# Kernel optimization log

Hardware: AMD Instinct MI355X
Metric: run time of the kernel (lower is better)

The kernel has to match this reference:

```python
import jax, jax.numpy as jnp
import numpy as np

N, E, DIN, ED, H, C = 50000, 800000, 128, 16, 4, 128
HC = H * C
SLOPE = 0.2


def gat_conv(x, ei_src, ei_dst, ea, W, a_src, a_dst, We, a_e, b):
    # x: [N, din]; ea: [E, ed] (self-loops already appended by caller)
    n = x.shape[0]
    h = (x @ W).reshape(n, H, C)                       # [N,H,C]
    al_src = (h * a_src).sum(-1)                       # [N,H]
    al_dst = (h * a_dst).sum(-1)                       # [N,H]
    e = (ea @ We).reshape(-1, H, C)                    # [E,H,C]
    al_e = (e * a_e).sum(-1)                           # [E,H]
    alpha = al_src[ei_src] + al_dst[ei_dst] + al_e     # [E,H]
    alpha = jnp.where(alpha > 0, alpha, SLOPE * alpha)  # LeakyReLU(0.2)
    # per-destination-node segment softmax (stable)
    amax = jax.ops.segment_max(alpha, ei_dst, num_segments=n)
    amax = jnp.where(jnp.isfinite(amax), amax, 0.0)
    ex = jnp.exp(alpha - amax[ei_dst])
    den = jax.ops.segment_sum(ex, ei_dst, num_segments=n)
    alpha = ex / (den[ei_dst] + 1e-16)                 # [E,H]
    msg = h[ei_src] * alpha[:, :, None]                # [E,H,C]
    out = jax.ops.segment_sum(msg, ei_dst, num_segments=n)  # [N,H,C]
    return out.reshape(n, HC) + b


def setup_inputs() -> dict:
    key = jax.random.key(0)
    ks = jax.random.split(key, 16)
    s = 0.05
    inp = {
        "x": jax.random.normal(ks[0], (N, DIN), jnp.float32),
        "edge_index": jax.random.randint(ks[1], (2, E), 0, N, jnp.int64),
        "edge_features": jax.random.normal(ks[2], (E, ED), jnp.float32),
        # layer 1 params
        "W1": jax.random.normal(ks[3], (DIN, HC), jnp.float32) * s,
        "att_src1": jax.random.normal(ks[4], (H, C), jnp.float32) * s,
        "att_dst1": jax.random.normal(ks[5], (H, C), jnp.float32) * s,
        "lin_e1": jax.random.normal(ks[6], (ED, HC), jnp.float32) * s,
        "att_e1": jax.random.normal(ks[7], (H, C), jnp.float32) * s,
        "b1": jnp.zeros((HC,), jnp.float32),
        # layer 2 params
        "W2": jax.random.normal(ks[8], (HC, HC), jnp.float32) * s,
        "att_src2": jax.random.normal(ks[9], (H, C), jnp.float32) * s,
        "att_dst2": jax.random.normal(ks[10], (H, C), jnp.float32) * s,
        "lin_e2": jax.random.normal(ks[11], (ED, HC), jnp.float32) * s,
        "att_e2": jax.random.normal(ks[12], (H, C), jnp.float32) * s,
        "b2": jnp.zeros((HC,), jnp.float32),
    }
    return inp


def reference(x, edge_index, edge_features,
              W1, att_src1, att_dst1, lin_e1, att_e1, b1,
              W2, att_src2, att_dst2, lin_e2, att_e2, b2):
    # add self-loops once (PyG default: add_self_loops=True, edge_attr fill='mean')
    loop = jnp.arange(N, dtype=edge_index.dtype)
    ei_src = jnp.concatenate([edge_index[0], loop])
    ei_dst = jnp.concatenate([edge_index[1], loop])
    mean_ea = edge_features.mean(0)
    ea = jnp.concatenate([edge_features, jnp.broadcast_to(mean_ea, (N, ED))], axis=0)

    h = gat_conv(x, ei_src, ei_dst, ea, W1, att_src1, att_dst1, lin_e1, att_e1, b1)
    h = jax.nn.elu(h)
    h = gat_conv(h, ei_src, ei_dst, ea, W2, att_src2, att_dst2, lin_e2, att_e2, b2)
    return jax.nn.elu(h)
```

## Files before the change

kernel.cpp:

```cpp
#include <hip/hip_runtime.h>
#include <math.h>

#define NNODE 50000
#define NEDGE 800000
#define DINv  128
#define EDv   16
#define NHv   4
#define CHv   128
#define HCv   512
#define SLOPEv 0.2f
#define MEANBLK 512
#define CONVN (NNODE * DINv / 4)

typedef __attribute__((ext_vector_type(8))) short bf16x8;
typedef __attribute__((ext_vector_type(4))) float f32x4;
typedef __attribute__((address_space(3))) unsigned lds_u32;
typedef const __attribute__((address_space(1))) unsigned glb_u32;

__device__ __forceinline__ ushort f2b(float f) {
  unsigned u = __float_as_uint(f);
  u += 0x7FFF + ((u >> 16) & 1);
  return (ushort)(u >> 16);
}
__device__ __forceinline__ float blo(unsigned u) { return __uint_as_float(u << 16); }
__device__ __forceinline__ float bhi(unsigned u) { return __uint_as_float(u & 0xffff0000u); }

__global__ void detect_kernel(const int* __restrict__ ei, int* __restrict__ flag) {
  __shared__ int bad;
  if (threadIdx.x == 0) bad = 0;
  __syncthreads();
  for (int i = threadIdx.x; i < 2048; i += 256)
    if (ei[2 * i + 1] != 0) bad = 1;
  __syncthreads();
  if (threadIdx.x == 0) flag[0] = bad ? 0 : 1;
}

__device__ __forceinline__ int load_idx(const int* __restrict__ ei, int e, int row, int wide) {
  if (wide) return ei[2 * ((size_t)row * NEDGE + e)];
  return ei[(size_t)row * NEDGE + e];
}

__global__ void count_kernel(const int* __restrict__ ei, const int* __restrict__ flag,
                             int* __restrict__ deg) {
  int e = blockIdx.x * blockDim.x + threadIdx.x;
  if (e < NEDGE) {
    int w = flag[0];
    atomicAdd(&deg[load_idx(ei, e, 1, w)], 1);
  }
}

__global__ __launch_bounds__(1024) void scan_kernel(const int* __restrict__ deg,
                                                    int* __restrict__ row_ptr) {
  __shared__ int wsum[16];
  int tid = threadIdx.x;
  int wid = tid >> 6, lane = tid & 63;
  int carry = 0;
  for (int base = 0; base < NNODE; base += 4096) {
    int idx = base + tid * 4;
    int4 x = make_int4(0, 0, 0, 0);
    if (idx < NNODE) x = *(const int4*)(deg + idx);
    int t0 = x.x, t1 = t0 + x.y, t2 = t1 + x.z, t3 = t2 + x.w;
    int v = t3;
#pragma unroll
    for (int off = 1; off < 64; off <<= 1) {
      int t = __shfl_up(v, off, 64);
      if (lane >= off) v += t;
    }
    if (lane == 63) wsum[wid] = v;
    __syncthreads();
    if (wid == 0) {
      int s = (lane < 16) ? wsum[lane] : 0;
#pragma unroll
      for (int off = 1; off < 16; off <<= 1) {
        int t = __shfl_up(s, off, 64);
        if (lane >= off) s += t;
      }
      if (lane < 16) wsum[lane] = s;
    }
    __syncthreads();
    int woff = wid ? wsum[wid - 1] : 0;
    int excl = carry + woff + v - t3;
    if (idx < NNODE) {
      int4 o = make_int4(excl, excl + t0, excl + t1, excl + t2);
      *(int4*)(row_ptr + idx) = o;
    }
    carry += wsum[15];
    __syncthreads();
  }
  if (tid == 0) row_ptr[NNODE] = carry;
}

__global__ void scatter_kernel(const int* __restrict__ ei, const int* __restrict__ flag,
                               const int* __restrict__ row_ptr, int* __restrict__ cursor,
                               int* __restrict__ src_sorted, int* __restrict__ pos) {
  int e = blockIdx.x * blockDim.x + threadIdx.x;
  if (e < NEDGE) {
    int w = flag[0];
    int d = load_idx(ei, e, 1, w);
    int s = load_idx(ei, e, 0, w);
    int p = row_ptr[d] + atomicAdd(&cursor[d], 1);
    src_sorted[p] = s;
    pos[e] = p;
  }
}

__global__ void prep_kernel(const float* __restrict__ We1, const float* __restrict__ ae1,
                            const float* __restrict__ We2, const float* __restrict__ ae2,
                            float* __restrict__ v1, float* __restrict__ v2) {
  int t = threadIdx.x;
  int layer = t >> 6, u = t & 63;
  int d = u >> 2, h = u & 3;
  const float* We = layer ? We2 : We1;
  const float* ae = layer ? ae2 : ae1;
  float s = 0.f;
  for (int c = 0; c < CHv; c++) s += We[(size_t)d * HCv + h * CHv + c] * ae[h * CHv + c];
  (layer ? v2 : v1)[d * 4 + h] = s;
}

__global__ void ale_both_kernel(const float* __restrict__ ea, const int* __restrict__ pos,
                                const float* __restrict__ v1, const float* __restrict__ v2,
                                float* __restrict__ al1, float* __restrict__ al2,
                                float* __restrict__ partials) {
  __shared__ float sv1[64], sv2[64];
  if (threadIdx.x < 64) sv1[threadIdx.x] = v1[threadIdx.x];
  else if (threadIdx.x < 128) sv2[threadIdx.x - 64] = v2[threadIdx.x - 64];
  __syncthreads();
  float acc[EDv];
#pragma unroll
  for (int d = 0; d < EDv; d++) acc[d] = 0.f;
  int stride = gridDim.x * blockDim.x;
  for (int e = blockIdx.x * blockDim.x + threadIdx.x; e < NEDGE; e += stride) {
    const float4* pr = (const float4*)(ea + (size_t)e * EDv);
    float row[16];
    *(float4*)&row[0] = pr[0]; *(float4*)&row[4] = pr[1];
    *(float4*)&row[8] = pr[2]; *(float4*)&row[12] = pr[3];
    float a0 = 0, a1 = 0, a2 = 0, a3 = 0;
    float b0 = 0, b1 = 0, b2 = 0, b3 = 0;
#pragma unroll
    for (int d = 0; d < 16; d++) {
      acc[d] += row[d];
      a0 += row[d] * sv1[d * 4 + 0];
      a1 += row[d] * sv1[d * 4 + 1];
      a2 += row[d] * sv1[d * 4 + 2];
      a3 += row[d] * sv1[d * 4 + 3];
      b0 += row[d] * sv2[d * 4 + 0];
      b1 += row[d] * sv2[d * 4 + 1];
      b2 += row[d] * sv2[d * 4 + 2];
      b3 += row[d] * sv2[d * 4 + 3];
    }
    int p = pos[e];
    ((float4*)al1)[p] = make_float4(a0, a1, a2, a3);
    ((float4*)al2)[p] = make_float4(b0, b1, b2, b3);
  }
  __shared__ float red[4][EDv];
  int wid = threadIdx.x >> 6, lane = threadIdx.x & 63;
#pragma unroll
  for (int d = 0; d < EDv; d++) {
    float v = acc[d];
    for (int off = 32; off; off >>= 1) v += __shfl_down(v, off, 64);
    if (lane == 0) red[wid][d] = v;
  }
  __syncthreads();
  if (threadIdx.x < EDv) {
    float v = red[0][threadIdx.x] + red[1][threadIdx.x] + red[2][threadIdx.x] + red[3][threadIdx.x];
    partials[blockIdx.x * EDv + threadIdx.x] = v;
  }
}

__global__ void fold_kernel(const float* __restrict__ partials,
                            const float* __restrict__ v1, const float* __restrict__ v2,
                            float* __restrict__ loop1, float* __restrict__ loop2) {
  int tid = threadIdx.x;
  int d = tid & 15, r0 = tid >> 4;
  float v = 0.f;
  for (int r = r0; r < MEANBLK; r += 16) v += partials[r * EDv + d];
  __shared__ float buf[256];
  __shared__ float ms[16];
  buf[tid] = v;
  __syncthreads();
  if (r0 < 8) buf[tid] += buf[tid + 128];
  __syncthreads();
  if (r0 < 4) buf[tid] += buf[tid + 64];
  __syncthreads();
  if (r0 < 2) buf[tid] += buf[tid + 32];
  __syncthreads();
  if (r0 == 0) ms[d] = (buf[tid] + buf[tid + 16]) * (1.0f / NEDGE);
  __syncthreads();
  if (tid < 8) {
    const float* vv = (tid >> 2) ? v2 : v1;
    int h = tid & 3;
    float a = 0.f;
    for (int d2 = 0; d2 < EDv; d2++) a += ms[d2] * vv[d2 * 4 + h];
    ((tid >> 2) ? loop2 : loop1)[h] = a;
  }
}

__global__ void convwt_kernel(const float* __restrict__ x, const float* __restrict__ W1,
                              const float* __restrict__ W2, ushort* __restrict__ xb,
                              ushort* __restrict__ Bt1, ushort* __restrict__ Bt2) {
  int i = blockIdx.x * 256 + threadIdx.x;
  if (i < CONVN) {
    float4 v = ((const float4*)x)[i];
    ushort4 o;
    o.x = f2b(v.x); o.y = f2b(v.y); o.z = f2b(v.z); o.w = f2b(v.w);
    ((ushort4*)xb)[i] = o;
  } else if (i < CONVN + DINv * HCv) {
    int idx = i - CONVN;
    int k = idx >> 9, n = idx & (HCv - 1);
    Bt1[(size_t)n * DINv + k] = f2b(W1[idx]);
  } else if (i < CONVN + DINv * HCv + HCv * HCv) {
    int idx = i - CONVN - DINv * HCv;
    int k = idx >> 9, n = idx & (HCv - 1);
    Bt2[(size_t)n * HCv + k] = f2b(W2[idx]);
  }
}

__global__ __launch_bounds__(256) void gemm_mfma_kernel(const ushort* __restrict__ A,
                                                        const ushort* __restrict__ Bt,
                                                        ushort* __restrict__ C, int M, int K,
                                                        const float* __restrict__ a_src,
                                                        const float* __restrict__ a_dst,
                                                        float* __restrict__ al_src,
                                                        float* __restrict__ al_dst) {
  __shared__ ushort As[8][128][8];
  __shared__ ushort Bs[8][128][8];
  __shared__ float ssa[128], ssd[128];
  __shared__ float rsum[2][128][2];
  int tid = threadIdx.x;
  int wid = tid >> 6, lane = tid & 63;

  int nblk = gridDim.x * gridDim.y;
  int j = blockIdx.y * gridDim.x + blockIdx.x;
  int q = nblk >> 3, rem = nblk & 7;
  int xcd = j & 7, idx = j >> 3;
  int d = (xcd < rem) ? xcd * (q + 1) + idx : rem * (q + 1) + (xcd - rem) * q + idx;
  int rb = (d >> 2) * 128, cb = (d & 3) * 128;
  int hblk = cb >> 7;

  int wm = (wid >> 1) * 64, wn = (wid & 1) * 64;
  int lr = lane & 15, lq = lane >> 4;

  if (tid < 128) { ssa[tid] = a_src[cb + tid]; ssd[tid] = a_dst[cb + tid]; }

  f32x4 acc[4][4];
#pragma unroll
  for (int i = 0; i < 4; i++)
#pragma unroll
    for (int jx = 0; jx < 4; jx++) acc[i][jx] = (f32x4){0.f, 0.f, 0.f, 0.f};

  ushort* AsF = &As[0][0][0];
  ushort* BsF = &Bs[0][0][0];

  for (int k0 = 0; k0 < K; k0 += 64) {
#pragma unroll
    for (int s = 0; s < 4; s++) {
      int c = s * 256 + tid;
      int kq = c >> 7, m = c & 127;
      int row = rb + m; if (row >= M) row = M - 1;
      const ushort* gA = A + (size_t)row * K + k0 + kq * 8;
      __builtin_amdgcn_global_load_lds((glb_u32*)gA, (lds_u32*)(AsF + (size_t)c * 8), 16, 0, 0);
    }
#pragma unroll
    for (int s = 0; s < 4; s++) {
      int c = s * 256 + tid;
      int kq = c >> 7, n = c & 127;
      const ushort* gB = Bt + (size_t)(cb + n) * K + k0 + kq * 8;
      __builtin_amdgcn_global_load_lds((glb_u32*)gB, (lds_u32*)(BsF + (size_t)c * 8), 16, 0, 0);
    }
    __syncthreads();
#pragma unroll
    for (int hh = 0; hh < 2; hh++) {
      bf16x8 af[4], bfr[4];
#pragma unroll
      for (int i = 0; i < 4; i++) {
        af[i]  = *(const bf16x8*)&As[hh * 4 + lq][wm + i * 16 + lr][0];
        bfr[i] = *(const bf16x8*)&Bs[hh * 4 + lq][wn + i * 16 + lr][0];
      }
#pragma unroll
      for (int i = 0; i < 4; i++)
#pragma unroll
        for (int jx = 0; jx < 4; jx++)
          acc[i][jx] = __builtin_amdgcn_mfma_f32_16x16x32_bf16(af[i], bfr[jx], acc[i][jx], 0, 0, 0);
    }
    __syncthreads();
  }

#pragma unroll
  for (int i = 0; i < 4; i++) {
    int rbase = rb + wm + i * 16 + lq * 4;
#pragma unroll
    for (int jx = 0; jx < 4; jx++) {
      int col = cb + wn + jx * 16 + lr;
#pragma unroll
      for (int r = 0; r < 4; r++) {
        int row = rbase + r;
        if (row < M) C[(size_t)row * HCv + col] = f2b(acc[i][jx][r]);
      }
    }
  }

  float sa[4], sd[4];
#pragma unroll
  for (int jx = 0; jx < 4; jx++) {
    int c = wn + jx * 16 + lr;
    sa[jx] = ssa[c]; sd[jx] = ssd[c];
  }
#pragma unroll
  for (int i = 0; i < 4; i++) {
#pragma unroll
    for (int r = 0; r < 4; r++) {
      float s1 = 0.f, s2 = 0.f;
#pragma unroll
      for (int jx = 0; jx < 4; jx++) {
        s1 = fmaf(acc[i][jx][r], sa[jx], s1);
        s2 = fmaf(acc[i][jx][r], sd[jx], s2);
      }
#pragma unroll
      for (int off = 1; off < 16; off <<= 1) {
        s1 += __shfl_xor(s1, off, 16);
        s2 += __shfl_xor(s2, off, 16);
      }
      if (lr == 0) {
        int row = wm + i * 16 + lq * 4 + r;
        rsum[0][row][wn >> 6] = s1;
        rsum[1][row][wn >> 6] = s2;
      }
    }
  }
  __syncthreads();
  if (tid < 128) {
    int row = rb + tid;
    if (row < M) {
      al_src[(size_t)row * 4 + hblk] = rsum[0][tid][0] + rsum[0][tid][1];
      al_dst[(size_t)row * 4 + hblk] = rsum[1][tid][0] + rsum[1][tid][1];
    }
  }
}

__device__ __forceinline__ void fma8(float* acc, float w, uint4 u) {
  acc[0] = fmaf(w, blo(u.x), acc[0]);
  acc[1] = fmaf(w, bhi(u.x), acc[1]);
  acc[2] = fmaf(w, blo(u.y), acc[2]);
  acc[3] = fmaf(w, bhi(u.y), acc[3]);
  acc[4] = fmaf(w, blo(u.z), acc[4]);
  acc[5] = fmaf(w, bhi(u.z), acc[5]);
  acc[6] = fmaf(w, blo(u.w), acc[6]);
  acc[7] = fmaf(w, bhi(u.w), acc[7]);
}

__global__ __launch_bounds__(256) void node_kernel(
    const ushort* __restrict__ hb, const float* __restrict__ al_src,
    const float* __restrict__ al_dst, const float* __restrict__ al_e,
    const float* __restrict__ loop_al_e, const int* __restrict__ row_ptr,
    const int* __restrict__ src_sorted, const float* __restrict__ bias,
    float* __restrict__ outf, ushort* __restrict__ outb) {
  int wid = threadIdx.x >> 6, lane = threadIdx.x & 63;
  int n = blockIdx.x * 4 + wid;
  if (n >= NNODE) return;
  int base = row_ptr[n];
  int deg = row_ptr[n + 1] - base;
  int h = lane >> 4;
  int jj = lane & 15;

  float aldh = al_dst[(size_t)n * 4 + h];
  float a0 = al_src[(size_t)n * 4 + h] + aldh + loop_al_e[h];
  float alph = a0 > 0.f ? a0 : SLOPEv * a0;
  float wl = __expf(alph);

  uint4 uself = *((const uint4*)(hb + ((size_t)n << 9)) + lane);

  float acc[8];
#pragma unroll
  for (int q = 0; q < 8; q++) acc[q] = 0.f;
  float den = 0.f;

  for (int cs = 0; cs < deg; cs += 16) {
    int cl = min(16, deg - cs);
    float w = 0.f;
    int sv = 0;
    if (jj < cl) {
      int p = base + cs + jj;
      sv = src_sorted[p];
      float a = al_src[(size_t)sv * 4 + h] + al_e[(size_t)p * 4 + h] + aldh;
      a = a > 0.f ? a : SLOPEv * a;
      w = __expf(a);
      den += w;
    }
    int cl4 = (cl + 3) & ~3;
    for (int j0 = 0; j0 < cl4; j0 += 4) {
      int s0 = __shfl(sv, j0 + 0, 16);
      int s1 = __shfl(sv, j0 + 1, 16);
      int s2 = __shfl(sv, j0 + 2, 16);
      int s3 = __shfl(sv, j0 + 3, 16);
      float w0 = __shfl(w, j0 + 0, 16);
      float w1 = __shfl(w, j0 + 1, 16);
      float w2 = __shfl(w, j0 + 2, 16);
      float w3 = __shfl(w, j0 + 3, 16);
      uint4 u0 = *((const uint4*)(hb + ((size_t)s0 << 9)) + lane);
      uint4 u1 = *((const uint4*)(hb + ((size_t)s1 << 9)) + lane);
      uint4 u2 = *((const uint4*)(hb + ((size_t)s2 << 9)) + lane);
      uint4 u3 = *((const uint4*)(hb + ((size_t)s3 << 9)) + lane);
      fma8(acc, w0, u0);
      fma8(acc, w1, u1);
      fma8(acc, w2, u2);
      fma8(acc, w3, u3);
    }
  }

  fma8(acc, wl, uself);

#pragma unroll
  for (int off = 8; off; off >>= 1) den += __shfl_xor(den, off, 16);
  den += wl;
  float rden = 1.f / (den + 1e-16f);

  const float4* bp = (const float4*)(bias + lane * 8);
  float4 b0 = bp[0], b1 = bp[1];
  float bv[8] = {b0.x, b0.y, b0.z, b0.w, b1.x, b1.y, b1.z, b1.w};
  float r[8];
#pragma unroll
  for (int q = 0; q < 8; q++) {
    float t = acc[q] * rden + bv[q];
    r[q] = t > 0.f ? t : expm1f(t);
  }
  if (outf) {
    float4* op = (float4*)(outf + (size_t)n * HCv + lane * 8);
    op[0] = make_float4(r[0], r[1], r[2], r[3]);
    op[1] = make_float4(r[4], r[5], r[6], r[7]);
  }
  if (outb) {
    uint4 o;
    o.x = (unsigned)f2b(r[0]) | ((unsigned)f2b(r[1]) << 16);
    o.y = (unsigned)f2b(r[2]) | ((unsigned)f2b(r[3]) << 16);
    o.z = (unsigned)f2b(r[4]) | ((unsigned)f2b(r[5]) << 16);
    o.w = (unsigned)f2b(r[6]) | ((unsigned)f2b(r[7]) << 16);
    ((uint4*)(outb + (size_t)n * HCv))[lane] = o;
  }
}

static inline char* take(char*& p, size_t bytes) {
  char* r = p;
  p += (bytes + 255) & ~(size_t)255;
  return r;
}

extern "C" void kernel_launch(void* const* d_in, const int* in_sizes, int n_in,
                              void* d_out, int out_size, void* d_ws, size_t ws_size,
                              hipStream_t stream) {
  (void)in_sizes; (void)n_in; (void)out_size; (void)ws_size;
  const float* x   = (const float*)d_in[0];
  const int*   ei  = (const int*)d_in[1];
  const float* ea  = (const float*)d_in[2];
  const float* W1  = (const float*)d_in[3];
  const float* as1 = (const float*)d_in[4];
  const float* ad1 = (const float*)d_in[5];
  const float* We1 = (const float*)d_in[6];
  const float* ae1 = (const float*)d_in[7];
  const float* b1  = (const float*)d_in[8];
  const float* W2  = (const float*)d_in[9];
  const float* as2 = (const float*)d_in[10];
  const float* ad2 = (const float*)d_in[11];
  const float* We2 = (const float*)d_in[12];
  const float* ae2 = (const float*)d_in[13];
  const float* b2  = (const float*)d_in[14];
  float* out = (float*)d_out;

  char* p = (char*)d_ws;
  ushort* hb        = (ushort*)take(p, (size_t)NNODE * HCv * 2);
  float* al_src     = (float*)take(p, (size_t)NNODE * 4 * 4);
  float* al_dst     = (float*)take(p, (size_t)NNODE * 4 * 4);
  float* ale1       = (float*)take(p, (size_t)NEDGE * 4 * 4);
  float* ale2       = (float*)take(p, (size_t)NEDGE * 4 * 4);
  int*   src_sorted = (int*)take(p, (size_t)NEDGE * 4);
  int*   pos        = (int*)take(p, (size_t)NEDGE * 4);
  int*   row_ptr    = (int*)take(p, (size_t)(NNODE + 1) * 4);
  float* partials   = (float*)take(p, (size_t)MEANBLK * EDv * 4);
  ushort* Bt1       = (ushort*)take(p, (size_t)HCv * DINv * 2);
  ushort* Bt2       = (ushort*)take(p, (size_t)HCv * HCv * 2);
  char* zero_begin = p;
  int*   deg        = (int*)take(p, (size_t)NNODE * 4);
  int*   cursor     = (int*)take(p, (size_t)NNODE * 4);
  size_t zero_len = (size_t)(p - zero_begin);
  float* v1         = (float*)take(p, 64 * 4);
  float* v2         = (float*)take(p, 64 * 4);
  float* loop1      = (float*)take(p, 4 * 4);
  float* loop2      = (float*)take(p, 4 * 4);
  int*   flag       = (int*)take(p, 4);

  ushort* xb  = (ushort*)d_out;
  ushort* h1b = (ushort*)((char*)d_out + (size_t)16 * 1024 * 1024);

  hipMemsetAsync(zero_begin, 0, zero_len, stream);

  detect_kernel<<<1, 256, 0, stream>>>(ei, flag);
  count_kernel<<<(NEDGE + 255) / 256, 256, 0, stream>>>(ei, flag, deg);
  scan_kernel<<<1, 1024, 0, stream>>>(deg, row_ptr);
  scatter_kernel<<<(NEDGE + 255) / 256, 256, 0, stream>>>(ei, flag, row_ptr, cursor,
                                                          src_sorted, pos);
  prep_kernel<<<1, 128, 0, stream>>>(We1, ae1, We2, ae2, v1, v2);
  convwt_kernel<<<(CONVN + DINv * HCv + HCv * HCv + 255) / 256, 256, 0, stream>>>(
      x, W1, W2, xb, Bt1, Bt2);
  ale_both_kernel<<<MEANBLK, 256, 0, stream>>>(ea, pos, v1, v2, ale1, ale2, partials);
  fold_kernel<<<1, 256, 0, stream>>>(partials, v1, v2, loop1, loop2);

  gemm_mfma_kernel<<<dim3(HCv / 128, (NNODE + 127) / 128), 256, 0, stream>>>(
      xb, Bt1, hb, NNODE, DINv, as1, ad1, al_src, al_dst);
  node_kernel<<<(NNODE + 3) / 4, 256, 0, stream>>>(hb, al_src, al_dst, ale1, loop1, row_ptr,
                                                   src_sorted, b1, (float*)nullptr, h1b);

  gemm_mfma_kernel<<<dim3(HCv / 128, (NNODE + 127) / 128), 256, 0, stream>>>(
      h1b, Bt2, hb, NNODE, HCv, as2, ad2, al_src, al_dst);
  node_kernel<<<(NNODE + 3) / 4, 256, 0, stream>>>(hb, al_src, al_dst, ale2, loop2, row_ptr,
                                                   src_sorted, b2, out, (ushort*)nullptr);
}
```

Baseline: 770.9 us.

## Precombine per-edge source and edge attention terms in sorted order before aggregation

The scatter now records the original edge id at each sorted position instead of the sorted position of each edge. New edge kernels add al_src[src] to the edge attention term in CSR order, so each node kernel reads one contiguous value per edge rather than a random al_src gather. The edge-feature mean is split into its own kernel. This adds two extra passes over all edges and a gather of edge features through eid_sorted, in exchange for removing scattered loads from the latency-bound node kernels.

```diff
diff --git a/kernel.cpp b/kernel.cpp
--- a/kernel.cpp
+++ b/kernel.cpp
@@ -92,7 +92,7 @@
 
 __global__ void scatter_kernel(const int* __restrict__ ei, const int* __restrict__ flag,
                                const int* __restrict__ row_ptr, int* __restrict__ cursor,
-                               int* __restrict__ src_sorted, int* __restrict__ pos) {
+                               int* __restrict__ src_sorted, int* __restrict__ eid_sorted) {
   int e = blockIdx.x * blockDim.x + threadIdx.x;
   if (e < NEDGE) {
     int w = flag[0];
@@ -100,7 +100,7 @@
     int s = load_idx(ei, e, 0, w);
     int p = row_ptr[d] + atomicAdd(&cursor[d], 1);
     src_sorted[p] = s;
-    pos[e] = p;
+    eid_sorted[p] = e;
   }
 }
 
@@ -117,40 +117,19 @@
   (layer ? v2 : v1)[d * 4 + h] = s;
 }
 
-__global__ void ale_both_kernel(const float* __restrict__ ea, const int* __restrict__ pos,
-                                const float* __restrict__ v1, const float* __restrict__ v2,
-                                float* __restrict__ al1, float* __restrict__ al2,
-                                float* __restrict__ partials) {
-  __shared__ float sv1[64], sv2[64];
-  if (threadIdx.x < 64) sv1[threadIdx.x] = v1[threadIdx.x];
-  else if (threadIdx.x < 128) sv2[threadIdx.x - 64] = v2[threadIdx.x - 64];
-  __syncthreads();
+__global__ void mean_part_kernel(const float* __restrict__ ea, float* __restrict__ partials) {
   float acc[EDv];
 #pragma unroll
   for (int d = 0; d < EDv; d++) acc[d] = 0.f;
   int stride = gridDim.x * blockDim.x;
-  for (int e = blockIdx.x * blockDim.x + threadIdx.x; e < NEDGE; e += stride) {
-    const float4* pr = (const float4*)(ea + (size_t)e * EDv);
-    float row[16];
-    *(float4*)&row[0] = pr[0]; *(float4*)&row[4] = pr[1];
-    *(float4*)&row[8] = pr[2]; *(float4*)&row[12] = pr[3];
-    float a0 = 0, a1 = 0, a2 = 0, a3 = 0;
-    float b0 = 0, b1 = 0, b2 = 0, b3 = 0;
-#pragma unroll
-    for (int d = 0; d < 16; d++) {
-      acc[d] += row[d];
-      a0 += row[d] * sv1[d * 4 + 0];
-      a1 += row[d] * sv1[d * 4 + 1];
-      a2 += row[d] * sv1[d * 4 + 2];
-      a3 += row[d] * sv1[d * 4 + 3];
-      b0 += row[d] * sv2[d * 4 + 0];
-      b1 += row[d] * sv2[d * 4 + 1];
-      b2 += row[d] * sv2[d * 4 + 2];
-      b3 += row[d] * sv2[d * 4 + 3];
-    }
-    int p = pos[e];
-    ((float4*)al1)[p] = make_float4(a0, a1, a2, a3);
-    ((float4*)al2)[p] = make_float4(b0, b1, b2, b3);
+  for (int r = blockIdx.x * blockDim.x + threadIdx.x; r < NEDGE; r += stride) {
+    const float4* p = (const float4*)(ea + (size_t)r * EDv);
+#pragma unroll
+    for (int q = 0; q < 4; q++) {
+      float4 v = p[q];
+      acc[q * 4 + 0] += v.x; acc[q * 4 + 1] += v.y;
+      acc[q * 4 + 2] += v.z; acc[q * 4 + 3] += v.w;
+    }
   }
   __shared__ float red[4][EDv];
   int wid = threadIdx.x >> 6, lane = threadIdx.x & 63;
@@ -215,6 +194,50 @@
   }
 }
 
+__global__ void apre1_kernel(const int* __restrict__ src_sorted, const int* __restrict__ eid_sorted,
+                             const float* __restrict__ ea, const float* __restrict__ al_src,
+                             const float* __restrict__ v1, const float* __restrict__ v2,
+                             float* __restrict__ ap1, float* __restrict__ ale2s) {
+  __shared__ float sv1[64], sv2[64];
+  if (threadIdx.x < 64) sv1[threadIdx.x] = v1[threadIdx.x];
+  else if (threadIdx.x < 128) sv2[threadIdx.x - 64] = v2[threadIdx.x - 64];
+  __syncthreads();
+  int p = blockIdx.x * 256 + threadIdx.x;
+  if (p >= NEDGE) return;
+  int s = src_sorted[p];
+  int e = eid_sorted[p];
+  const float4* pr = (const float4*)(ea + (size_t)e * EDv);
+  float row[16];
+  *(float4*)&row[0] = pr[0]; *(float4*)&row[4] = pr[1];
+  *(float4*)&row[8] = pr[2]; *(float4*)&row[12] = pr[3];
+  float a0 = 0, a1 = 0, a2 = 0, a3 = 0;
+  float b0 = 0, b1 = 0, b2 = 0, b3 = 0;
+#pragma unroll
+  for (int d = 0; d < 16; d++) {
+    a0 += row[d] * sv1[d * 4 + 0];
+    a1 += row[d] * sv1[d * 4 + 1];
+    a2 += row[d] * sv1[d * 4 + 2];
+    a3 += row[d] * sv1[d * 4 + 3];
+    b0 += row[d] * sv2[d * 4 + 0];
+    b1 += row[d] * sv2[d * 4 + 1];
+    b2 += row[d] * sv2[d * 4 + 2];
+    b3 += row[d] * sv2[d * 4 + 3];
+  }
+  float4 as = ((const float4*)al_src)[s];
+  ((float4*)ap1)[p] = make_float4(as.x + a0, as.y + a1, as.z + a2, as.w + a3);
+  ((float4*)ale2s)[p] = make_float4(b0, b1, b2, b3);
+}
+
+__global__ void apre2_kernel(const int* __restrict__ src_sorted, const float* __restrict__ ale2s,
+                             const float* __restrict__ al_src, float* __restrict__ ap2) {
+  int p = blockIdx.x * 256 + threadIdx.x;
+  if (p >= NEDGE) return;
+  int s = src_sorted[p];
+  float4 a = ((const float4*)al_src)[s];
+  float4 b = ((const float4*)ale2s)[p];
+  ((float4*)ap2)[p] = make_float4(a.x + b.x, a.y + b.y, a.z + b.z, a.w + b.w);
+}
+
 __global__ __launch_bounds__(256) void gemm_mfma_kernel(const ushort* __restrict__ A,
                                                         const ushort* __restrict__ Bt,
                                                         ushort* __restrict__ C, int M, int K,
@@ -350,7 +373,7 @@
 
 __global__ __launch_bounds__(256) void node_kernel(
     const ushort* __restrict__ hb, const float* __restrict__ al_src,
-    const float* __restrict__ al_dst, const float* __restrict__ al_e,
+    const float* __restrict__ al_dst, const float* __restrict__ ap,
     const float* __restrict__ loop_al_e, const int* __restrict__ row_ptr,
     const int* __restrict__ src_sorted, const float* __restrict__ bias,
     float* __restrict__ outf, ushort* __restrict__ outb) {
@@ -381,7 +404,7 @@
     if (jj < cl) {
       int p = base + cs + jj;
       sv = src_sorted[p];
-      float a = al_src[(size_t)sv * 4 + h] + al_e[(size_t)p * 4 + h] + aldh;
+      float a = ap[(size_t)p * 4 + h] + aldh;
       a = a > 0.f ? a : SLOPEv * a;
       w = __expf(a);
       den += w;
@@ -469,10 +492,10 @@
   ushort* hb        = (ushort*)take(p, (size_t)NNODE * HCv * 2);
   float* al_src     = (float*)take(p, (size_t)NNODE * 4 * 4);
   float* al_dst     = (float*)take(p, (size_t)NNODE * 4 * 4);
-  float* ale1       = (float*)take(p, (size_t)NEDGE * 4 * 4);
-  float* ale2       = (float*)take(p, (size_t)NEDGE * 4 * 4);
+  float* ap         = (float*)take(p, (size_t)NEDGE * 4 * 4);
+  float* ale2s      = (float*)take(p, (size_t)NEDGE * 4 * 4);
   int*   src_sorted = (int*)take(p, (size_t)NEDGE * 4);
-  int*   pos        = (int*)take(p, (size_t)NEDGE * 4);
+  int*   eid_sorted = (int*)take(p, (size_t)NEDGE * 4);
   int*   row_ptr    = (int*)take(p, (size_t)(NNODE + 1) * 4);
   float* partials   = (float*)take(p, (size_t)MEANBLK * EDv * 4);
   ushort* Bt1       = (ushort*)take(p, (size_t)HCv * DINv * 2);
@@ -496,20 +519,23 @@
   count_kernel<<<(NEDGE + 255) / 256, 256, 0, stream>>>(ei, flag, deg);
   scan_kernel<<<1, 1024, 0, stream>>>(deg, row_ptr);
   scatter_kernel<<<(NEDGE + 255) / 256, 256, 0, stream>>>(ei, flag, row_ptr, cursor,
-                                                          src_sorted, pos);
+                                                          src_sorted, eid_sorted);
   prep_kernel<<<1, 128, 0, stream>>>(We1, ae1, We2, ae2, v1, v2);
+  mean_part_kernel<<<MEANBLK, 256, 0, stream>>>(ea, partials);
+  fold_kernel<<<1, 256, 0, stream>>>(partials, v1, v2, loop1, loop2);
   convwt_kernel<<<(CONVN + DINv * HCv + HCv * HCv + 255) / 256, 256, 0, stream>>>(
       x, W1, W2, xb, Bt1, Bt2);
-  ale_both_kernel<<<MEANBLK, 256, 0, stream>>>(ea, pos, v1, v2, ale1, ale2, partials);
-  fold_kernel<<<1, 256, 0, stream>>>(partials, v1, v2, loop1, loop2);
 
   gemm_mfma_kernel<<<dim3(HCv / 128, (NNODE + 127) / 128), 256, 0, stream>>>(
       xb, Bt1, hb, NNODE, DINv, as1, ad1, al_src, al_dst);
-  node_kernel<<<(NNODE + 3) / 4, 256, 0, stream>>>(hb, al_src, al_dst, ale1, loop1, row_ptr,
+  apre1_kernel<<<(NEDGE + 255) / 256, 256, 0, stream>>>(src_sorted, eid_sorted, ea, al_src,
+                                                        v1, v2, ap, ale2s);
+  node_kernel<<<(NNODE + 3) / 4, 256, 0, stream>>>(hb, al_src, al_dst, ap, loop1, row_ptr,
                                                    src_sorted, b1, (float*)nullptr, h1b);
 
   gemm_mfma_kernel<<<dim3(HCv / 128, (NNODE + 127) / 128), 256, 0, stream>>>(
       h1b, Bt2, hb, NNODE, HCv, as2, ad2, al_src, al_dst);
-  node_kernel<<<(NNODE + 3) / 4, 256, 0, stream>>>(hb, al_src, al_dst, ale2, loop2, row_ptr,
+  apre2_kernel<<<(NEDGE + 255) / 256, 256, 0, stream>>>(src_sorted, ale2s, al_src, ap);
+  node_kernel<<<(NNODE + 3) / 4, 256, 0, stream>>>(hb, al_src, al_dst, ap, loop2, row_ptr,
                                                    src_sorted, b2, out, (ushort*)nullptr);
 }
```

Result: faster. 720.8 us (-6.5%).
